# Optimization experiments

Hardware: AMD Instinct MI355X
Metric: run time of the kernel (lower is better)

Reference implementation:

```python
import jax, jax.numpy as jnp
import numpy as np
from jax import lax

V, E, H, F = 30000, 256, 512, 2048
B, S = 64, 20
HW = 49  # 7*7 spatial locations


def setup_inputs() -> dict:
    key = jax.random.key(0)
    ks = jax.random.split(key, 24)
    s = 0.02
    emb = jax.random.normal(ks[3], (V, E), jnp.float32) * s
    emb = emb.at[0].set(0.0)  # padding_idx=0
    G = 4 * H
    return {
        "word_ids": jax.random.randint(ks[0], (B, S), 0, V),
        "cnn_feat": jax.random.normal(ks[1], (B, H), jnp.float32),
        "attn_enhanced_feat": jax.random.normal(ks[2], (B, F, 7, 7), jnp.float32),
        "embed_table": emb,
        "Wf": jax.random.normal(ks[4], (H, F), jnp.float32) * s,
        "bf": jnp.zeros((H,), jnp.float32),
        "Wa": jax.random.normal(ks[5], (H, H), jnp.float32) * s,
        "ba": jnp.zeros((H,), jnp.float32),
        "W_ih0": jax.random.normal(ks[6], (G, E + H), jnp.float32) * s,
        "W_hh0": jax.random.normal(ks[7], (G, H), jnp.float32) * s,
        "b_ih0": jnp.zeros((G,), jnp.float32),
        "b_hh0": jnp.zeros((G,), jnp.float32),
        "W_ih1": jax.random.normal(ks[8], (G, H), jnp.float32) * s,
        "W_hh1": jax.random.normal(ks[9], (G, H), jnp.float32) * s,
        "b_ih1": jnp.zeros((G,), jnp.float32),
        "b_hh1": jnp.zeros((G,), jnp.float32),
        "W_hi": jax.random.normal(ks[10], (H, H), jnp.float32) * s,
        "b_hi": jnp.zeros((H,), jnp.float32),
        "W_ci": jax.random.normal(ks[11], (H, H), jnp.float32) * s,
        "b_ci": jnp.zeros((H,), jnp.float32),
        "W_out": jax.random.normal(ks[12], (V, H), jnp.float32) * s,
        "b_out": jnp.zeros((V,), jnp.float32),
    }


def _lstm_cell(x, h, c, Wih, Whh, bih, bhh):
    # torch nn.LSTM gate order: i, f, g, o
    gates = x @ Wih.T + bih + h @ Whh.T + bhh
    i, f, g, o = jnp.split(gates, 4, axis=-1)
    i, f, o = jax.nn.sigmoid(i), jax.nn.sigmoid(f), jax.nn.sigmoid(o)
    g = jnp.tanh(g)
    c_new = f * c + i * g
    h_new = o * jnp.tanh(c_new)
    return h_new, c_new


def reference(word_ids, cnn_feat, attn_enhanced_feat, embed_table, Wf, bf, Wa, ba,
              W_ih0, W_hh0, b_ih0, b_hh0, W_ih1, W_hh1, b_ih1, b_hh1,
              W_hi, b_hi, W_ci, b_ci, W_out, b_out):
    b = word_ids.shape[0]
    # init hidden/cell (same tanh-projected vector replicated to both layers)
    h_init = jnp.tanh(cnn_feat @ W_hi.T + b_hi)
    c_init = jnp.tanh(cnn_feat @ W_ci.T + b_ci)
    # loop-invariant feature projection: (B, 49, H) — computed once
    feat = attn_enhanced_feat.reshape(b, F, HW).transpose(0, 2, 1)  # (B,49,F)
    proj = feat @ Wf.T + bf  # (B,49,H)
    # embedding with padding_idx=0 semantics
    emb = embed_table[word_ids] * (word_ids != 0)[..., None].astype(embed_table.dtype)
    xs = emb.transpose(1, 0, 2)  # (S,B,E)

    def step(carry, x_t):
        h0, c0, h1, c1 = carry
        ha = h1 @ Wa.T + ba                                   # (B,H)
        scores = jnp.einsum('bh,bph->bp', ha, proj)            # (B,49)
        w = jax.nn.softmax(scores, axis=1)
        ctx = jnp.einsum('bp,bph->bh', w, proj)                # (B,H)
        xin = jnp.concatenate([x_t, ctx], axis=1)              # (B,E+H)
        h0n, c0n = _lstm_cell(xin, h0, c0, W_ih0, W_hh0, b_ih0, b_hh0)
        h1n, c1n = _lstm_cell(h0n, h1, c1, W_ih1, W_hh1, b_ih1, b_hh1)
        out = h1n @ W_out.T + b_out                            # (B,V)
        return (h0n, c0n, h1n, c1n), out

    (h0, c0, h1, c1), outs = lax.scan(step, (h_init, c_init, h_init, c_init), xs)
    outputs = outs.transpose(1, 0, 2)  # (B,S,V)
    h_final = jnp.stack([h0, h1], axis=0)  # (2,B,H)
    c_final = jnp.stack([c0, c1], axis=0)
    return outputs, h_final, c_final
```

## Files before the change

kernel.cpp:

```cpp
#include <hip/hip_runtime.h>
#include <hip/hip_bf16.h>

typedef long long i64;

#define NB   64
#define NS   20
#define NV   30000
#define NE   256
#define NH   512
#define NF   2048
#define NP   49
#define NG   2048

typedef __attribute__((ext_vector_type(8))) __bf16 bf16x8;
typedef __attribute__((ext_vector_type(4))) float  f32x4;

__device__ __forceinline__ float sigm(float x) { return 1.f / (1.f + expf(-x)); }

__device__ __forceinline__ void gload_lds16(const void* g, void* l) {
    __builtin_amdgcn_global_load_lds(
        (const __attribute__((address_space(1))) void*)g,
        (__attribute__((address_space(3))) void*)l, 16, 0, 0);
}

__global__ __launch_bounds__(256) void init_hc(
    const float* __restrict__ cnn, const float* __restrict__ Whi, const float* __restrict__ bhi,
    const float* __restrict__ Wci, const float* __restrict__ bci,
    float* __restrict__ xa, float* __restrict__ xb, float* __restrict__ c0, float* __restrict__ c1)
{
    int b = blockIdx.x, tid = threadIdx.x;
    __shared__ float xsh[NH];
    xsh[tid] = cnn[(i64)b * NH + tid];
    xsh[tid + 256] = cnn[(i64)b * NH + 256 + tid];
    __syncthreads();
    #pragma unroll
    for (int hh = 0; hh < 2; hh++) {
        int h = tid + hh * 256;
        const float4* wh = (const float4*)(Whi + (i64)h * NH);
        const float4* wc = (const float4*)(Wci + (i64)h * NH);
        const float4* xv = (const float4*)xsh;
        float ah = bhi[h], ac = bci[h];
        for (int k = 0; k < NH / 4; k++) {
            float4 x = xv[k], a = wh[k], c = wc[k];
            ah += a.x * x.x + a.y * x.y + a.z * x.z + a.w * x.w;
            ac += c.x * x.x + c.y * x.y + c.z * x.z + c.w * x.w;
        }
        float th = tanhf(ah), tc = tanhf(ac);
        xa[(i64)b * 1024 + 512 + h] = th;
        xb[(i64)b * 1024 + 512 + h] = th;
        c0[(i64)b * NH + h] = tc;
        c1[(i64)b * NH + h] = tc;
    }
}

__global__ __launch_bounds__(256) void embed_kernel(
    const int* __restrict__ ids, const float* __restrict__ table, float* __restrict__ xs)
{
    int blk = blockIdx.x;
    int t = blk / NB, b = blk % NB;
    int id = ids[(i64)b * NS + t];
    float v = (id == 0) ? 0.f : table[(i64)id * NE + threadIdx.x];
    xs[(i64)blk * NE + threadIdx.x] = v;
}

__global__ __launch_bounds__(256) void cast_bf16_kernel(
    const float* __restrict__ in, __hip_bfloat16* __restrict__ outp, int n8)
{
    int i = blockIdx.x * 256 + threadIdx.x;
    if (i >= n8) return;
    const float4* p = (const float4*)(in + (i64)i * 8);
    float4 a = p[0], b = p[1];
    __hip_bfloat16 v[8];
    v[0] = __float2bfloat16(a.x); v[1] = __float2bfloat16(a.y);
    v[2] = __float2bfloat16(a.z); v[3] = __float2bfloat16(a.w);
    v[4] = __float2bfloat16(b.x); v[5] = __float2bfloat16(b.y);
    v[6] = __float2bfloat16(b.z); v[7] = __float2bfloat16(b.w);
    *(float4*)(outp + (i64)i * 8) = *(float4*)v;
}

__global__ __launch_bounds__(256) void proj_kernel(
    const float* __restrict__ af, const float* __restrict__ Wf,
    const float* __restrict__ bf, float* __restrict__ proj)
{
    __shared__ float As[16][132];
    __shared__ float Bs[16][68];
    const int tid = threadIdx.x;
    const int bn = blockIdx.x * 64;
    const int bm = blockIdx.y * 128;
    const int tn = (tid & 15) * 4, tm = (tid >> 4) * 8;
    const int lk = tid & 15, lr = tid >> 4;
    const int lm = tid & 127, lkq = tid >> 7;
    const int m_g = bm + lm;
    const int bA = m_g / NP, pA = m_g - bA * NP;
    float acc[8][4] = {};
    for (int k0 = 0; k0 < NF; k0 += 16) {
        #pragma unroll
        for (int i = 0; i < 8; i++) {
            int kk = lkq * 8 + i;
            As[kk][lm] = (m_g < NB * NP) ? af[(i64)bA * (NF * NP) + (i64)(k0 + kk) * NP + pA] : 0.f;
        }
        #pragma unroll
        for (int i = 0; i < 4; i++) {
            int n = bn + lr + i * 16;
            Bs[lk][lr + i * 16] = Wf[(i64)n * NF + k0 + lk];
        }
        __syncthreads();
        #pragma unroll
        for (int kk = 0; kk < 16; kk++) {
            float a[8], bv[4];
            #pragma unroll
            for (int i = 0; i < 8; i++) a[i] = As[kk][tm + i];
            #pragma unroll
            for (int j = 0; j < 4; j++) bv[j] = Bs[kk][tn + j];
            #pragma unroll
            for (int i = 0; i < 8; i++)
                #pragma unroll
                for (int j = 0; j < 4; j++) acc[i][j] += a[i] * bv[j];
        }
        __syncthreads();
    }
    #pragma unroll
    for (int i = 0; i < 8; i++) {
        int m = bm + tm + i;
        if (m < NB * NP) {
            #pragma unroll
            for (int j = 0; j < 4; j++) {
                int n = bn + tn + j;
                proj[(i64)m * NH + n] = acc[i][j] + bf[n];
            }
        }
    }
}

struct GArgs {
    const float* A; i64 lda;
    const float* Bm; i64 ldb;
    const float* bias1; const float* bias2;
    float* C; i64 ldc;
    int M, N, K, outmode;
};

__global__ __launch_bounds__(256) void gemm128_kernel(GArgs g)
{
    __shared__ float As[16][132];
    __shared__ float Bs[16][68];
    const int tid = threadIdx.x;
    const int bn = blockIdx.x * 64;
    const int bm = blockIdx.y * 128;
    const int tn = (tid & 15) * 4, tm = (tid >> 4) * 8;
    const int lk = tid & 15, lr = tid >> 4;
    float acc[8][4] = {};
    for (int k0 = 0; k0 < g.K; k0 += 16) {
        #pragma unroll
        for (int i = 0; i < 8; i++) {
            int m = bm + lr + i * 16;
            As[lk][lr + i * 16] = (m < g.M) ? g.A[(i64)m * g.lda + k0 + lk] : 0.f;
        }
        #pragma unroll
        for (int i = 0; i < 4; i++) {
            int n = bn + lr + i * 16;
            Bs[lk][lr + i * 16] = (n < g.N) ? g.Bm[(i64)n * g.ldb + k0 + lk] : 0.f;
        }
        __syncthreads();
        #pragma unroll
        for (int kk = 0; kk < 16; kk++) {
            float a[8], bv[4];
            #pragma unroll
            for (int i = 0; i < 8; i++) a[i] = As[kk][tm + i];
            #pragma unroll
            for (int j = 0; j < 4; j++) bv[j] = Bs[kk][tn + j];
            #pragma unroll
            for (int i = 0; i < 8; i++)
                #pragma unroll
                for (int j = 0; j < 4; j++) acc[i][j] += a[i] * bv[j];
        }
        __syncthreads();
    }
    #pragma unroll
    for (int i = 0; i < 8; i++) {
        int m = bm + tm + i;
        if (m >= g.M) continue;
        int n0 = bn + tn;
        float v[4];
        #pragma unroll
        for (int j = 0; j < 4; j++) {
            v[j] = acc[i][j];
            int n = n0 + j;
            if (n < g.N) {
                if (g.bias1) v[j] += g.bias1[n];
                if (g.bias2) v[j] += g.bias2[n];
            }
        }
        i64 base = g.outmode ? (i64)(m & 63) * ((i64)NS * NV) + (i64)(m >> 6) * NV + n0
                             : (i64)m * g.ldc + n0;
        if (n0 + 3 < g.N) {
            *(float4*)&g.C[base] = make_float4(v[0], v[1], v[2], v[3]);
        } else {
            #pragma unroll
            for (int j = 0; j < 4; j++)
                if (n0 + j < g.N) g.C[base + j] = v[j];
        }
    }
}

__global__ __launch_bounds__(256) void gemm_out_mfma(
    const __hip_bfloat16* __restrict__ Ab_, const __hip_bfloat16* __restrict__ Wb_,
    const float* __restrict__ bout, float* __restrict__ out)
{
    __shared__ __bf16 As[128 * 64];
    __shared__ __bf16 Bs[128 * 64];
    const __bf16* Ab = (const __bf16*)Ab_;
    const __bf16* Wb = (const __bf16*)Wb_;

    int orig = blockIdx.x;
    int xcd = orig & 7, local = orig >> 3;
    int wgid = (xcd < 6 ? xcd * 294 : 6 * 294 + (xcd - 6) * 293) + local;
    const int bn = (wgid / 10) * 128;
    const int bm = (wgid % 10) * 128;

    const int tid = threadIdx.x;
    const int w = tid >> 6;
    const int l = tid & 63;
    const int wr = w >> 1, wc = w & 1;

    f32x4 acc[4][4] = {};

    for (int k0 = 0; k0 < NH; k0 += 64) {
        #pragma unroll
        for (int r = 0; r < 4; r++) {
            int rowA = r * 32 + w * 8 + (l >> 3);
            const __bf16* srcA = Ab + (i64)(bm + rowA) * NH + k0 + (l & 7) * 8;
            gload_lds16(srcA, &As[(r * 32 + w * 8) * 64]);
            int rowBn = bn + r * 32 + w * 8 + (l >> 3);
            if (rowBn >= NV) rowBn = 0;
            const __bf16* srcB = Wb + (i64)rowBn * NH + k0 + (l & 7) * 8;
            gload_lds16(srcB, &Bs[(r * 32 + w * 8) * 64]);
        }
        __syncthreads();
        #pragma unroll
        for (int kk = 0; kk < 2; kk++) {
            bf16x8 af[4], bfr[4];
            #pragma unroll
            for (int mr = 0; mr < 4; mr++)
                af[mr] = *(const bf16x8*)&As[(wr * 64 + mr * 16 + (l & 15)) * 64 + kk * 32 + (l >> 4) * 8];
            #pragma unroll
            for (int nr = 0; nr < 4; nr++)
                bfr[nr] = *(const bf16x8*)&Bs[(wc * 64 + nr * 16 + (l & 15)) * 64 + kk * 32 + (l >> 4) * 8];
            #pragma unroll
            for (int mr = 0; mr < 4; mr++)
                #pragma unroll
                for (int nr = 0; nr < 4; nr++)
                    acc[mr][nr] = __builtin_amdgcn_mfma_f32_16x16x32_bf16(af[mr], bfr[nr], acc[mr][nr], 0, 0, 0);
        }
        __syncthreads();
    }

    #pragma unroll
    for (int nr = 0; nr < 4; nr++) {
        int n = bn + wc * 64 + nr * 16 + (l & 15);
        if (n >= NV) continue;
        float bv = bout[n];
        #pragma unroll
        for (int mr = 0; mr < 4; mr++) {
            int mbase = bm + wr * 64 + mr * 16 + (l >> 4) * 4;
            #pragma unroll
            for (int j = 0; j < 4; j++) {
                int m = mbase + j;
                out[(i64)(m & 63) * ((i64)NS * NV) + (i64)(m >> 6) * NV + n] = acc[mr][nr][j] + bv;
            }
        }
    }
}

__global__ __launch_bounds__(256) void attn_fused(
    const float* __restrict__ gpart,
    const float* __restrict__ bih1, const float* __restrict__ bhh1,
    float* __restrict__ c1, float* __restrict__ xb,
    float* __restrict__ h1f, __hip_bfloat16* __restrict__ h1b,
    const float* __restrict__ Wa, const float* __restrict__ ba,
    const float* __restrict__ proj, float* __restrict__ xa)
{
    int b = blockIdx.x, tid = threadIdx.x;
    __shared__ float h1s[NH];
    __shared__ float has[NH];
    __shared__ float sw[64];
    if (gpart) {
        #pragma unroll
        for (int hh = 0; hh < 2; hh++) {
            int h = tid + hh * 256;
            float gi = bih1[h] + bhh1[h];
            float gf = bih1[h + 512] + bhh1[h + 512];
            float gg = bih1[h + 1024] + bhh1[h + 1024];
            float go = bih1[h + 1536] + bhh1[h + 1536];
            #pragma unroll
            for (int z = 0; z < 8; z++) {
                const float* gp = gpart + ((i64)z * NB + b) * NG;
                gi += gp[h]; gf += gp[h + 512]; gg += gp[h + 1024]; go += gp[h + 1536];
            }
            float i = sigm(gi), f = sigm(gf), g2 = tanhf(gg), o = sigm(go);
            float c = f * c1[(i64)b * NH + h] + i * g2;
            c1[(i64)b * NH + h] = c;
            float hn = o * tanhf(c);
            h1s[h] = hn;
            xb[(i64)b * 1024 + 512 + h] = hn;
            if (h1f) h1f[(i64)b * NH + h] = hn;
            if (h1b) h1b[(i64)b * NH + h] = __float2bfloat16(hn);
        }
    } else {
        h1s[tid] = xb[(i64)b * 1024 + 512 + tid];
        h1s[tid + 256] = xb[(i64)b * 1024 + 768 + tid];
    }
    __syncthreads();
    #pragma unroll
    for (int hh = 0; hh < 2; hh++) {
        int h = tid + hh * 256;
        const float4* w4 = (const float4*)(Wa + (i64)h * NH);
        const float4* h4 = (const float4*)h1s;
        float acc = ba[h];
        for (int k = 0; k < NH / 4; k++) {
            float4 a = w4[k], x = h4[k];
            acc += a.x * x.x + a.y * x.y + a.z * x.z + a.w * x.w;
        }
        has[h] = acc;
    }
    __syncthreads();
    int wv = tid >> 6, ln = tid & 63;
    for (int p = wv; p < NP; p += 4) {
        const float* pp = proj + ((i64)b * NP + p) * NH;
        float s = 0.f;
        #pragma unroll
        for (int j = 0; j < NH / 64; j++) s += has[ln + j * 64] * pp[ln + j * 64];
        #pragma unroll
        for (int off = 32; off > 0; off >>= 1) s += __shfl_down(s, off, 64);
        if (ln == 0) sw[p] = s;
    }
    __syncthreads();
    if (tid < 64) {
        float v = (tid < NP) ? sw[tid] : -3.4e38f;
        float m = v;
        #pragma unroll
        for (int off = 32; off > 0; off >>= 1) m = fmaxf(m, __shfl_xor(m, off, 64));
        float e = (tid < NP) ? expf(v - m) : 0.f;
        float s = e;
        #pragma unroll
        for (int off = 32; off > 0; off >>= 1) s += __shfl_xor(s, off, 64);
        if (tid < NP) sw[tid] = e / s;
    }
    __syncthreads();
    #pragma unroll
    for (int hh = 0; hh < 2; hh++) {
        int h = tid + hh * 256;
        float acc = 0.f;
        for (int p = 0; p < NP; p++) acc += sw[p] * proj[((i64)b * NP + p) * NH + h];
        xa[(i64)b * 1024 + h] = acc;
    }
}

struct LArgs {
    const float* A;
    const float* B1; i64 ldb1; int bo1;
    const float* B2; i64 ldb2;
    float* gpart;
};

__global__ __launch_bounds__(256) void lstm_gemm_kernel(LArgs g)
{
    __shared__ float As[16][68];
    __shared__ float Bs[16][68];
    const int tid = threadIdx.x;
    const int bn = blockIdx.x * 64;
    const int kz = blockIdx.z;
    const int tn = (tid & 15) * 4, tm = (tid >> 4) * 4;
    const int lk = tid & 15, lr = tid >> 4;
    float acc[4][4] = {};
    for (int k0 = kz * 128; k0 < kz * 128 + 128; k0 += 16) {
        #pragma unroll
        for (int i = 0; i < 4; i++) {
            int m = lr + i * 16;
            As[lk][lr + i * 16] = g.A[(i64)m * 1024 + k0 + lk];
        }
        int k = k0 + lk;
        const float* bp = (k < 512) ? (g.B1 + g.bo1 + k) : (g.B2 + (k - 512));
        i64 ldb = (k < 512) ? g.ldb1 : g.ldb2;
        #pragma unroll
        for (int i = 0; i < 4; i++) {
            int n = bn + lr + i * 16;
            Bs[lk][lr + i * 16] = bp[(i64)n * ldb];
        }
        __syncthreads();
        #pragma unroll
        for (int kk = 0; kk < 16; kk++) {
            float a[4], bv[4];
            #pragma unroll
            for (int i = 0; i < 4; i++) a[i] = As[kk][tm + i];
            #pragma unroll
            for (int j = 0; j < 4; j++) bv[j] = Bs[kk][tn + j];
            #pragma unroll
            for (int i = 0; i < 4; i++)
                #pragma unroll
                for (int j = 0; j < 4; j++) acc[i][j] += a[i] * bv[j];
        }
        __syncthreads();
    }
    float* out = g.gpart + (i64)kz * NB * NG;
    #pragma unroll
    for (int i = 0; i < 4; i++) {
        *(float4*)&out[(i64)(tm + i) * NG + bn + tn] =
            make_float4(acc[i][0], acc[i][1], acc[i][2], acc[i][3]);
    }
}

__global__ __launch_bounds__(512) void lstm_fin_kernel(
    const float* __restrict__ gpart, const float* __restrict__ xpre_t,
    const float* __restrict__ bih, const float* __restrict__ bhh,
    float* __restrict__ cbuf, float* __restrict__ hA, float* __restrict__ hB,
    float* __restrict__ h1f, __hip_bfloat16* __restrict__ h1b)
{
    int b = blockIdx.x, h = threadIdx.x;
    float gi, gf, gg, go;
    if (xpre_t) {
        const float* xp = xpre_t + (i64)b * NG;
        gi = xp[h]; gf = xp[h + 512]; gg = xp[h + 1024]; go = xp[h + 1536];
    } else {
        gi = bih[h] + bhh[h];
        gf = bih[h + 512] + bhh[h + 512];
        gg = bih[h + 1024] + bhh[h + 1024];
        go = bih[h + 1536] + bhh[h + 1536];
    }
    #pragma unroll
    for (int z = 0; z < 8; z++) {
        const float* gp = gpart + ((i64)z * NB + b) * NG;
        gi += gp[h]; gf += gp[h + 512]; gg += gp[h + 1024]; go += gp[h + 1536];
    }
    float i = sigm(gi), f = sigm(gf), g2 = tanhf(gg), o = sigm(go);
    float c = f * cbuf[(i64)b * NH + h] + i * g2;
    cbuf[(i64)b * NH + h] = c;
    float hn = o * tanhf(c);
    hA[(i64)b * 1024 + h] = hn;
    if (hB) hB[(i64)b * 1024 + h] = hn;
    if (h1f) h1f[(i64)b * NH + h] = hn;
    if (h1b) h1b[(i64)b * NH + h] = __float2bfloat16(hn);
}

__global__ __launch_bounds__(512) void final_copy(
    const float* __restrict__ xb, const float* __restrict__ c0, const float* __restrict__ c1,
    float* __restrict__ out)
{
    int b = blockIdx.x, h = threadIdx.x;
    const i64 OB = (i64)NB * NS * NV;
    out[OB + (i64)b * NH + h] = xb[(i64)b * 1024 + h];
    out[OB + (i64)NB * NH + (i64)b * NH + h] = xb[(i64)b * 1024 + 512 + h];
    out[OB + 2 * (i64)NB * NH + (i64)b * NH + h] = c0[(i64)b * NH + h];
    out[OB + 3 * (i64)NB * NH + (i64)b * NH + h] = c1[(i64)b * NH + h];
}

extern "C" void kernel_launch(void* const* d_in, const int* in_sizes, int n_in,
                              void* d_out, int out_size, void* d_ws, size_t ws_size,
                              hipStream_t stream)
{
    (void)in_sizes; (void)n_in; (void)out_size;
    const int*   word_ids = (const int*)d_in[0];
    const float* cnn   = (const float*)d_in[1];
    const float* attnf = (const float*)d_in[2];
    const float* table = (const float*)d_in[3];
    const float* Wf    = (const float*)d_in[4];
    const float* bfp   = (const float*)d_in[5];
    const float* Wa    = (const float*)d_in[6];
    const float* ba    = (const float*)d_in[7];
    const float* Wih0  = (const float*)d_in[8];
    const float* Whh0  = (const float*)d_in[9];
    const float* bih0  = (const float*)d_in[10];
    const float* bhh0  = (const float*)d_in[11];
    const float* Wih1  = (const float*)d_in[12];
    const float* Whh1  = (const float*)d_in[13];
    const float* bih1  = (const float*)d_in[14];
    const float* bhh1  = (const float*)d_in[15];
    const float* Whi   = (const float*)d_in[16];
    const float* bhi   = (const float*)d_in[17];
    const float* Wci   = (const float*)d_in[18];
    const float* bci   = (const float*)d_in[19];
    const float* Wout  = (const float*)d_in[20];
    const float* bout  = (const float*)d_in[21];
    float* out = (float*)d_out;

    float* ws    = (float*)d_ws;
    float* proj  = ws;
    float* xs    = proj + 1605632;
    float* xpre  = xs + 327680;
    float* xa    = xpre + 2621440;
    float* xb    = xa + 65536;
    float* c0    = xb + 65536;
    float* c1    = c0 + 32768;
    float* gpart = c1 + 32768;
    float* tail  = gpart + 1048576;
    const i64 need_floats = 5799936 + 327680  + 7680000 ;
    bool use_mfma = ws_size >= (size_t)need_floats * 4;
    __hip_bfloat16* h1b   = (__hip_bfloat16*)tail;
    __hip_bfloat16* Woutb = (__hip_bfloat16*)(tail + 327680);
    float* h1f = tail;

    init_hc<<<dim3(NB), dim3(256), 0, stream>>>(cnn, Whi, bhi, Wci, bci, xa, xb, c0, c1);
    proj_kernel<<<dim3(8, 25), dim3(256), 0, stream>>>(attnf, Wf, bfp, proj);
    embed_kernel<<<dim3(NS * NB), dim3(256), 0, stream>>>(word_ids, table, xs);
    if (use_mfma)
        cast_bf16_kernel<<<dim3(7500), dim3(256), 0, stream>>>(Wout, Woutb, NV * NH / 8);

    GArgs gx{xs, NE, Wih0, NE + NH, bih0, bhh0, xpre, NG, NS * NB, NG, NE, 0};
    gemm128_kernel<<<dim3(NG / 64, 10), dim3(256), 0, stream>>>(gx);

    float*          h1f_arg = use_mfma ? nullptr : h1f;
    __hip_bfloat16* h1b_arg = use_mfma ? h1b : nullptr;

    for (int t = 0; t < NS; t++) {
        attn_fused<<<dim3(NB), dim3(256), 0, stream>>>(
            t ? gpart : (const float*)nullptr, bih1, bhh1, c1, xb,
            t ? (h1f_arg ? h1f_arg + (i64)(t - 1) * NB * NH : nullptr) : nullptr,
            t ? (h1b_arg ? h1b_arg + (i64)(t - 1) * NB * NH : nullptr) : nullptr,
            Wa, ba, proj, xa);
        LArgs l0{xa, Wih0, NE + NH, NE, Whh0, NH, gpart};
        lstm_gemm_kernel<<<dim3(NG / 64, 1, 8), dim3(256), 0, stream>>>(l0);
        lstm_fin_kernel<<<dim3(NB), dim3(512), 0, stream>>>(
            gpart, xpre + (i64)t * NB * NG, (const float*)nullptr, (const float*)nullptr,
            c0, xb, xa + 512, (float*)nullptr, (__hip_bfloat16*)nullptr);
        LArgs l1{xb, Wih1, NH, 0, Whh1, NH, gpart};
        lstm_gemm_kernel<<<dim3(NG / 64, 1, 8), dim3(256), 0, stream>>>(l1);
    }
    lstm_fin_kernel<<<dim3(NB), dim3(512), 0, stream>>>(
        gpart, (const float*)nullptr, bih1, bhh1,
        c1, xb + 512, (float*)nullptr,
        h1f_arg ? h1f_arg + (i64)(NS - 1) * NB * NH : nullptr,
        h1b_arg ? h1b_arg + (i64)(NS - 1) * NB * NH : nullptr);

    if (use_mfma) {
        gemm_out_mfma<<<dim3(2350), dim3(256), 0, stream>>>(h1b, Woutb, bout, out);
    } else {
        GArgs go{h1f, NH, Wout, NH, bout, nullptr, out, NV, NS * NB, NV, NH, 1};
        gemm128_kernel<<<dim3((NV + 63) / 64, 10), dim3(256), 0, stream>>>(go);
    }

    final_copy<<<dim3(NB), dim3(512), 0, stream>>>(xb, c0, c1, out);
}
```

Before: 1.927 ms.

## Compute feature projection with bf16 MFMA after transposing and casting inputs

Replaces the fp32 SIMT projection GEMM (3136x512x2048) with a path that first transposes and casts the attention features to bf16, casts Wf to bf16, and then runs an MFMA tiled GEMM. Workspace is rearranged so the transposed features and Wf copy share the region later reused for the bf16 W_out. This removes the scalar FMA cost of the projection but adds extra transpose and cast passes and lowers the precision of proj to bf16 inputs. The MFMA GEMM launches only 100 workgroups, which may underfill the device.

Measured after the change: 1.637 ms. 15.0% less time.

```diff
diff --git a/kernel.cpp b/kernel.cpp
--- a/kernel.cpp
+++ b/kernel.cpp
@@ -11,6 +11,7 @@
 #define NF   2048
 #define NP   49
 #define NG   2048
+#define NM   3136
 
 typedef __attribute__((ext_vector_type(8))) __bf16 bf16x8;
 typedef __attribute__((ext_vector_type(4))) float  f32x4;
@@ -76,6 +77,82 @@
     v[4] = __float2bfloat16(b.x); v[5] = __float2bfloat16(b.y);
     v[6] = __float2bfloat16(b.z); v[7] = __float2bfloat16(b.w);
     *(float4*)(outp + (i64)i * 8) = *(float4*)v;
+}
+
+__global__ __launch_bounds__(256) void tcast_kernel(
+    const float* __restrict__ af, __hip_bfloat16* __restrict__ featT)
+{
+    int b = blockIdx.x >> 5;
+    int f0 = (blockIdx.x & 31) * 64;
+    __shared__ float t[64][51];
+    int tid = threadIdx.x;
+    for (int idx = tid; idx < 64 * NP; idx += 256) {
+        int f = idx / NP, p = idx - f * NP;
+        t[f][p] = af[((i64)b * NF + f0 + f) * NP + p];
+    }
+    __syncthreads();
+    for (int idx = tid; idx < NP * 64; idx += 256) {
+        int p = idx >> 6, f = idx & 63;
+        featT[((i64)b * NP + p) * NF + f0 + f] = __float2bfloat16(t[f][p]);
+    }
+}
+
+__global__ __launch_bounds__(256) void proj_mfma(
+    const __hip_bfloat16* __restrict__ At_, const __hip_bfloat16* __restrict__ Wb_,
+    const float* __restrict__ bf, float* __restrict__ proj)
+{
+    __shared__ __bf16 As[128 * 64];
+    __shared__ __bf16 Bs[128 * 64];
+    const __bf16* At = (const __bf16*)At_;
+    const __bf16* Wb = (const __bf16*)Wb_;
+    const int wgid = blockIdx.x;
+    const int bm = (wgid % 25) * 128;
+    const int bn = (wgid / 25) * 128;
+    const int tid = threadIdx.x;
+    const int w = tid >> 6, l = tid & 63;
+    const int wr = w >> 1, wc = w & 1;
+    f32x4 acc[4][4] = {};
+    for (int k0 = 0; k0 < NF; k0 += 64) {
+        #pragma unroll
+        for (int r = 0; r < 4; r++) {
+            int rowA = bm + r * 32 + w * 8 + (l >> 3);
+            if (rowA >= NM) rowA = 0;
+            gload_lds16(At + (i64)rowA * NF + k0 + (l & 7) * 8, &As[(r * 32 + w * 8) * 64]);
+            int rowB = bn + r * 32 + w * 8 + (l >> 3);
+            gload_lds16(Wb + (i64)rowB * NF + k0 + (l & 7) * 8, &Bs[(r * 32 + w * 8) * 64]);
+        }
+        __syncthreads();
+        #pragma unroll
+        for (int kk = 0; kk < 2; kk++) {
+            bf16x8 af[4], bfr[4];
+            #pragma unroll
+            for (int mr = 0; mr < 4; mr++)
+                af[mr] = *(const bf16x8*)&As[(wr * 64 + mr * 16 + (l & 15)) * 64 + kk * 32 + (l >> 4) * 8];
+            #pragma unroll
+            for (int nr = 0; nr < 4; nr++)
+                bfr[nr] = *(const bf16x8*)&Bs[(wc * 64 + nr * 16 + (l & 15)) * 64 + kk * 32 + (l >> 4) * 8];
+            #pragma unroll
+            for (int mr = 0; mr < 4; mr++)
+                #pragma unroll
+                for (int nr = 0; nr < 4; nr++)
+                    acc[mr][nr] = __builtin_amdgcn_mfma_f32_16x16x32_bf16(af[mr], bfr[nr], acc[mr][nr], 0, 0, 0);
+        }
+        __syncthreads();
+    }
+    #pragma unroll
+    for (int nr = 0; nr < 4; nr++) {
+        int n = bn + wc * 64 + nr * 16 + (l & 15);
+        float bv = bf[n];
+        #pragma unroll
+        for (int mr = 0; mr < 4; mr++) {
+            int mbase = bm + wr * 64 + mr * 16 + (l >> 4) * 4;
+            #pragma unroll
+            for (int j = 0; j < 4; j++) {
+                int m = mbase + j;
+                if (m < NM) proj[(i64)m * NH + n] = acc[mr][nr][j] + bv;
+            }
+        }
+    }
 }
 
 __global__ __launch_bounds__(256) void proj_kernel(
@@ -97,7 +174,7 @@
         #pragma unroll
         for (int i = 0; i < 8; i++) {
             int kk = lkq * 8 + i;
-            As[kk][lm] = (m_g < NB * NP) ? af[(i64)bA * (NF * NP) + (i64)(k0 + kk) * NP + pA] : 0.f;
+            As[kk][lm] = (m_g < NM) ? af[(i64)bA * (NF * NP) + (i64)(k0 + kk) * NP + pA] : 0.f;
         }
         #pragma unroll
         for (int i = 0; i < 4; i++) {
@@ -122,7 +199,7 @@
     #pragma unroll
     for (int i = 0; i < 8; i++) {
         int m = bm + tm + i;
-        if (m < NB * NP) {
+        if (m < NM) {
             #pragma unroll
             for (int j = 0; j < 4; j++) {
                 int n = bn + tn + j;
@@ -211,20 +288,16 @@
     __shared__ __bf16 Bs[128 * 64];
     const __bf16* Ab = (const __bf16*)Ab_;
     const __bf16* Wb = (const __bf16*)Wb_;
-
     int orig = blockIdx.x;
     int xcd = orig & 7, local = orig >> 3;
     int wgid = (xcd < 6 ? xcd * 294 : 6 * 294 + (xcd - 6) * 293) + local;
     const int bn = (wgid / 10) * 128;
     const int bm = (wgid % 10) * 128;
-
     const int tid = threadIdx.x;
     const int w = tid >> 6;
     const int l = tid & 63;
     const int wr = w >> 1, wc = w & 1;
-
     f32x4 acc[4][4] = {};
-
     for (int k0 = 0; k0 < NH; k0 += 64) {
         #pragma unroll
         for (int r = 0; r < 4; r++) {
@@ -254,7 +327,6 @@
         }
         __syncthreads();
     }
-
     #pragma unroll
     for (int nr = 0; nr < 4; nr++) {
         int n = bn + wc * 64 + nr * 16 + (l & 15);
@@ -492,19 +564,28 @@
     float* c0    = xb + 65536;
     float* c1    = c0 + 32768;
     float* gpart = c1 + 32768;
-    float* tail  = gpart + 1048576;
-    const i64 need_floats = 5799936 + 327680  + 7680000 ;
+    float* h1bf  = gpart + 1048576;
+    float* tail  = h1bf + 655360;
+    const i64 need_floats = 6455296 + 7680000;
     bool use_mfma = ws_size >= (size_t)need_floats * 4;
-    __hip_bfloat16* h1b   = (__hip_bfloat16*)tail;
-    __hip_bfloat16* Woutb = (__hip_bfloat16*)(tail + 327680);
-    float* h1f = tail;
+    __hip_bfloat16* h1b   = (__hip_bfloat16*)h1bf;
+    __hip_bfloat16* featT = (__hip_bfloat16*)tail;
+    __hip_bfloat16* Wfb   = (__hip_bfloat16*)(tail + 3211264);
+    __hip_bfloat16* Woutb = (__hip_bfloat16*)tail;
+    float* h1f = h1bf;
 
     init_hc<<<dim3(NB), dim3(256), 0, stream>>>(cnn, Whi, bhi, Wci, bci, xa, xb, c0, c1);
-    proj_kernel<<<dim3(8, 25), dim3(256), 0, stream>>>(attnf, Wf, bfp, proj);
+
+    if (use_mfma) {
+        tcast_kernel<<<dim3(NB * 32), dim3(256), 0, stream>>>(attnf, featT);
+        cast_bf16_kernel<<<dim3(512), dim3(256), 0, stream>>>(Wf, Wfb, NH * NF / 8);
+        proj_mfma<<<dim3(100), dim3(256), 0, stream>>>(featT, Wfb, bfp, proj);
+        cast_bf16_kernel<<<dim3(7500), dim3(256), 0, stream>>>(Wout, Woutb, NV * NH / 8);
+    } else {
+        proj_kernel<<<dim3(8, 25), dim3(256), 0, stream>>>(attnf, Wf, bfp, proj);
+    }
+
     embed_kernel<<<dim3(NS * NB), dim3(256), 0, stream>>>(word_ids, table, xs);
-    if (use_mfma)
-        cast_bf16_kernel<<<dim3(7500), dim3(256), 0, stream>>>(Wout, Woutb, NV * NH / 8);
-
     GArgs gx{xs, NE, Wih0, NE + NH, bih0, bhh0, xpre, NG, NS * NB, NG, NE, 0};
     gemm128_kernel<<<dim3(NG / 64, 10), dim3(256), 0, stream>>>(gx);
 
```
